# Performance work log

Measured on AMD Instinct MI355X. Metric: run time of the kernel, lower is better.

## Reference

```python
import jax, jax.numpy as jnp
import numpy as np

B, S, D = 2, 1024, 4096
HQ, HKV, HD = 32, 8, 128
GROUPS = HQ // HKV          # 4
SCALE = HD ** -0.5


def _rope_tables(key):
    # standard RoPE cos/sin tables, non-interleaved (half-split) layout
    inv_freq = 1.0 / (10000.0 ** (jnp.arange(0, HD, 2, dtype=jnp.float32) / HD))  # [HD/2]
    pos = jnp.arange(S, dtype=jnp.float32)                                        # [S]
    freqs = pos[:, None] * inv_freq[None, :]                                      # [S, HD/2]
    emb = jnp.concatenate([freqs, freqs], axis=-1)                                # [S, HD]
    cos = jnp.broadcast_to(jnp.cos(emb)[None], (B, S, HD))
    sin = jnp.broadcast_to(jnp.sin(emb)[None], (B, S, HD))
    return cos, sin


def setup_inputs() -> dict:
    key = jax.random.key(0)
    ks = jax.random.split(key, 6)
    hidden_states = jax.random.normal(ks[0], (B, S, D), dtype=jnp.float32)
    cos_table, sin_table = _rope_tables(ks[1])
    Wq = jax.random.normal(ks[2], (D, HQ * HD), dtype=jnp.float32) * (D ** -0.5)
    Wk = jax.random.normal(ks[3], (D, HKV * HD), dtype=jnp.float32) * (D ** -0.5)
    Wv = jax.random.normal(ks[4], (D, HKV * HD), dtype=jnp.float32) * (D ** -0.5)
    Wo = jax.random.normal(ks[5], (HQ * HD, D), dtype=jnp.float32) * ((HQ * HD) ** -0.5)
    return {"hidden_states": hidden_states, "cos_table": cos_table,
            "sin_table": sin_table, "Wq": Wq, "Wk": Wk, "Wv": Wv, "Wo": Wo}


def _rotate_half(x):
    x1, x2 = jnp.split(x, 2, axis=-1)
    return jnp.concatenate([-x2, x1], axis=-1)


def _apply_rope(x, cos, sin):
    # x: [B, S, H, HD]; cos/sin: [B, S, HD] broadcast across heads
    c = cos[:, :, None, :]
    s = sin[:, :, None, :]
    return x * c + _rotate_half(x) * s


def reference(hidden_states, cos_table, sin_table, Wq, Wk, Wv, Wo):
    b, s, _ = hidden_states.shape
    # QKV projections (no bias, Llama-style)
    q = (hidden_states @ Wq).reshape(b, s, HQ, HD)
    k = (hidden_states @ Wk).reshape(b, s, HKV, HD)
    v = (hidden_states @ Wv).reshape(b, s, HKV, HD)
    # fused RoPE on q and k (in [B, S, H, HD] layout, as in source)
    q = _apply_rope(q, cos_table, sin_table)
    k = _apply_rope(k, cos_table, sin_table)
    # -> [B, H, S, HD]
    q = q.transpose(0, 2, 1, 3)
    k = k.transpose(0, 2, 1, 3)
    v = v.transpose(0, 2, 1, 3)
    # GQA repeat_kv: [B, HKV, S, HD] -> [B, HQ, S, HD]
    k = jnp.repeat(k, GROUPS, axis=1)
    v = jnp.repeat(v, GROUPS, axis=1)
    # SDPA, no mask (source calls sdpa without a mask)
    scores = jnp.einsum('bhqd,bhkd->bhqk', q, k) * SCALE
    attn = jax.nn.softmax(scores, axis=-1)
    out = jnp.einsum('bhqk,bhkd->bhqd', attn, v)
    out = out.transpose(0, 2, 1, 3).reshape(b, s, HQ * HD)
    return out @ Wo
```

## Files before the change

### kernel.cpp

```cpp
#include <hip/hip_runtime.h>

#define B_   2
#define S_   1024
#define D_   4096
#define HQ_  32
#define HKV_ 8
#define HD_  128
#define SCALE_ 0.08838834764831845f

typedef unsigned short u16;
typedef __attribute__((ext_vector_type(8))) short s16x8;
typedef __attribute__((ext_vector_type(4))) short s16x4;
typedef __attribute__((ext_vector_type(4))) float f32x4;

#define MFMA(a,b,c) __builtin_amdgcn_mfma_f32_16x16x32_bf16((a),(b),(c),0,0,0)

__device__ __forceinline__ u16 bf16_rne(float x) {
  unsigned u = __float_as_uint(x);
  u += 0x7fffu + ((u >> 16) & 1u);
  return (u16)(u >> 16);
}
__device__ __forceinline__ float bf16_up(u16 h) {
  return __uint_as_float(((unsigned)h) << 16);
}
__device__ __forceinline__ void split2(float x, u16& h, u16& l) {
  h = bf16_rne(x);
  l = bf16_rne(x - bf16_up(h));
}

__device__ __forceinline__ void cvt_hi_lo(float a, float b, unsigned& hi, unsigned& lo) {
  unsigned h, l;
  asm("v_cvt_pk_bf16_f32 %0, %1, %2" : "=v"(h) : "v"(a), "v"(b));
  float ra = __uint_as_float(h << 16);
  float rb = __uint_as_float(h & 0xffff0000u);
  float la = a - ra, lb = b - rb;
  asm("v_cvt_pk_bf16_f32 %0, %1, %2" : "=v"(l) : "v"(la), "v"(lb));
  hi = h; lo = l;
}
__device__ __forceinline__ void pack8(float4 x, float4 y, uint4& h, uint4& l) {
  unsigned h0,h1,h2,h3,l0,l1,l2,l3;
  cvt_hi_lo(x.x, x.y, h0, l0);
  cvt_hi_lo(x.z, x.w, h1, l1);
  cvt_hi_lo(y.x, y.y, h2, l2);
  cvt_hi_lo(y.z, y.w, h3, l3);
  h = make_uint4(h0,h1,h2,h3); l = make_uint4(l0,l1,l2,l3);
}

typedef const __attribute__((address_space(1))) void* gas_ptr;
typedef __attribute__((address_space(3))) void* las_ptr;
__device__ __forceinline__ void gload_lds16(const void* g, void* l) {
  __builtin_amdgcn_global_load_lds((gas_ptr)g, (las_ptr)l, 16, 0, 0);
}

__global__ __launch_bounds__(256) void frag_b(
    const float* __restrict__ W, u16* __restrict__ dh, u16* __restrict__ dl,
    int N, int n0, int Nc16)
{
  __shared__ float T[32][68];
  const int kt = blockIdx.x, nbk = blockIdx.y;
  const int tid = threadIdx.x;
#pragma unroll
  for (int rep = 0; rep < 2; ++rep) {
    int idx = tid + rep * 256;
    int row = idx >> 4, c4 = (idx & 15) * 4;
    float4 v = *reinterpret_cast<const float4*>(&W[(size_t)(kt*32 + row) * N + n0 + nbk*64 + c4]);
    *reinterpret_cast<float4*>(&T[row][c4]) = v;
  }
  __syncthreads();
  const size_t base = ((size_t)kt * Nc16 + nbk * 4) * 512;
  int c = tid;
  int nt = c >> 6, l = c & 63, kc = l >> 4, r = l & 15;
  u16 hh[8], ll[8];
#pragma unroll
  for (int j = 0; j < 8; ++j) split2(T[kc*8 + j][nt*16 + r], hh[j], ll[j]);
  *reinterpret_cast<s16x8*>(&dh[base + (size_t)c * 8]) =
    (s16x8){(short)hh[0],(short)hh[1],(short)hh[2],(short)hh[3],
            (short)hh[4],(short)hh[5],(short)hh[6],(short)hh[7]};
  *reinterpret_cast<s16x8*>(&dl[base + (size_t)c * 8]) =
    (s16x8){(short)ll[0],(short)ll[1],(short)ll[2],(short)ll[3],
            (short)ll[4],(short)ll[5],(short)ll[6],(short)ll[7]};
}

__global__ __launch_bounds__(512) void gemm_p1(
    const float* __restrict__ X, const float* __restrict__ abp,
    const u16* __restrict__ WF,
    float* __restrict__ qb, float* __restrict__ kb, float* __restrict__ vb,
    float* __restrict__ outp, int mode, int col0)
{
  __shared__ __attribute__((aligned(16))) u16 lds[40960];
  u16* ah0 = lds;
  u16* al0 = lds + 4096;
  u16* ah1 = lds + 8192;
  u16* al1 = lds + 12288;
  u16* bh0 = lds + 16384;
  u16* bh1 = lds + 24576;
  u16* blb = lds + 32768;

  const int id   = blockIdx.x;
  const int cpx  = gridDim.x >> 3;
  const int swz  = (id & 7) * cpx + (id >> 3);

  const float* A; const u16* Bh; const u16* Bl; float* C;
  int ldc, Nc16, mb, nb;
  if (mode == 0) {
    if (swz < 128)      { A=X; Bh=WF;          Bl=WF+8388608;  C=qb; ldc=4096; Nc16=128; mb=swz>>3; nb=swz&7; }
    else if (swz < 192) { int u=swz-128; A=X; Bh=WF+16777216; Bl=WF+20971520; C=kb; ldc=1024; Nc16=64; mb=u>>2; nb=u&3; }
    else                { int u=swz-192; A=X; Bh=WF+25165824; Bl=WF+29360128; C=vb; ldc=1024; Nc16=64; mb=u>>2; nb=u&3; }
  } else if (mode == 1) {
    A=X; Bh=WF; Bl=WF+8388608; C=qb+col0; ldc=4096; Nc16=128; mb=swz>>3; nb=swz&7;
  } else if (mode == 2) {
    if (swz < 64) { A=X; Bh=WF;          Bl=WF+4194304;  C=kb; ldc=1024; Nc16=64; mb=swz>>2; nb=swz&3; }
    else          { int u=swz-64; A=X; Bh=WF+8388608; Bl=WF+12582912; C=vb; ldc=1024; Nc16=64; mb=u>>2; nb=u&3; }
  } else if (mode == 3) {
    A=abp; Bh=WF; Bl=WF+16777216; C=outp; ldc=4096; Nc16=256; mb=swz>>4; nb=swz&15;
  } else {
    A=abp; Bh=WF; Bl=WF+8388608; C=outp+col0; ldc=4096; Nc16=128; mb=swz>>3; nb=swz&7;
  }

  const int tid  = threadIdx.x;
  const int lane = tid & 63;
  const int wid  = tid >> 6;
  const int mtb  = (wid >> 2) * 4;
  const int ntb  = (wid & 3) * 4;
  const int loff = lane * 8;

  const int arow = tid >> 2;
  const int akc  = tid & 3;
  const float* aptr = A + (size_t)(mb*128 + arow) * 4096 + akc*8;
  const int awr = (arow >> 4)*512 + (akc*16 + (arow & 15))*8;

  const size_t bStep = (size_t)Nc16 * 512;
  const u16* pBh = Bh + (size_t)nb*16*512 + loff;
  const u16* pBl = Bl + (size_t)nb*16*512 + loff;

  f32x4 acc[4][4];
#pragma unroll
  for (int i = 0; i < 4; ++i)
#pragma unroll
    for (int j = 0; j < 4; ++j) acc[i][j] = (f32x4){0.f, 0.f, 0.f, 0.f};

  float4 ra0 = *reinterpret_cast<const float4*>(aptr);
  float4 ra1 = *reinterpret_cast<const float4*>(aptr + 4);
  {
    uint4 h4, l4; pack8(ra0, ra1, h4, l4);
    *reinterpret_cast<uint4*>(&ah0[awr]) = h4;
    *reinterpret_cast<uint4*>(&al0[awr]) = l4;
  }
  gload_lds16(pBh + (size_t)wid*512,     bh0 + wid*512);
  gload_lds16(pBh + (size_t)(wid+8)*512, bh0 + (wid+8)*512);
  ra0 = *reinterpret_cast<const float4*>(aptr + 32);
  ra1 = *reinterpret_cast<const float4*>(aptr + 36);
  __syncthreads();

  for (int kt = 0; kt < 128; ++kt) {
    u16* cAh = (kt & 1) ? ah1 : ah0;
    u16* cAl = (kt & 1) ? al1 : al0;
    u16* nAh = (kt & 1) ? ah0 : ah1;
    u16* nAl = (kt & 1) ? al0 : al1;
    u16* cBh = (kt & 1) ? bh1 : bh0;
    u16* nBh = (kt & 1) ? bh0 : bh1;

    gload_lds16(pBl + (size_t)kt*bStep + (size_t)wid*512,     blb + wid*512);
    gload_lds16(pBl + (size_t)kt*bStep + (size_t)(wid+8)*512, blb + (wid+8)*512);
    if (kt < 127) {
      gload_lds16(pBh + (size_t)(kt+1)*bStep + (size_t)wid*512,     nBh + wid*512);
      gload_lds16(pBh + (size_t)(kt+1)*bStep + (size_t)(wid+8)*512, nBh + (wid+8)*512);
    }
    s16x8 a_h[4], a_l[4], b_h[4];
#pragma unroll
    for (int mf = 0; mf < 4; ++mf) {
      a_h[mf] = *reinterpret_cast<const s16x8*>(&cAh[(mtb+mf)*512 + loff]);
      a_l[mf] = *reinterpret_cast<const s16x8*>(&cAl[(mtb+mf)*512 + loff]);
    }
#pragma unroll
    for (int nf = 0; nf < 4; ++nf)
      b_h[nf] = *reinterpret_cast<const s16x8*>(&cBh[(ntb+nf)*512 + loff]);
#pragma unroll
    for (int mf = 0; mf < 4; ++mf)
#pragma unroll
      for (int nf = 0; nf < 4; ++nf) {
        acc[mf][nf] = MFMA(a_h[mf], b_h[nf], acc[mf][nf]);
        acc[mf][nf] = MFMA(a_l[mf], b_h[nf], acc[mf][nf]);
      }
    __syncthreads();

    s16x8 b_l[4];
#pragma unroll
    for (int nf = 0; nf < 4; ++nf)
      b_l[nf] = *reinterpret_cast<const s16x8*>(&blb[(ntb+nf)*512 + loff]);
#pragma unroll
    for (int mf = 0; mf < 4; ++mf)
#pragma unroll
      for (int nf = 0; nf < 4; ++nf)
        acc[mf][nf] = MFMA(a_h[mf], b_l[nf], acc[mf][nf]);
    if (kt < 127) {
      uint4 h4, l4; pack8(ra0, ra1, h4, l4);
      *reinterpret_cast<uint4*>(&nAh[awr]) = h4;
      *reinterpret_cast<uint4*>(&nAl[awr]) = l4;
      if (kt < 126) {
        ra0 = *reinterpret_cast<const float4*>(aptr + (kt+2)*32);
        ra1 = *reinterpret_cast<const float4*>(aptr + (kt+2)*32 + 4);
      }
    }
    __syncthreads();
  }

  const int lr = lane & 15, lg = lane >> 4;
  const int row0 = mb*128 + (wid >> 2) * 64;
  const int nloc = nb*256 + (wid & 3) * 64;
#pragma unroll
  for (int mf = 0; mf < 4; ++mf)
#pragma unroll
    for (int nf = 0; nf < 4; ++nf)
#pragma unroll
      for (int r = 0; r < 4; ++r)
        C[(size_t)(row0 + mf*16 + lg*4 + r) * ldc + nloc + nf*16 + lr] = acc[mf][nf][r];
}

__device__ __forceinline__ void gemm_core_128x256(
    const float* __restrict__ A, const float* __restrict__ W,
    float* __restrict__ C, int ldw, int m0, int n0)
{
  __shared__ u16 Ah[128][40];
  __shared__ u16 Al[128][40];
  __shared__ u16 Bh[256][40];
  __shared__ u16 Bl[256][40];

  const int tid  = threadIdx.x;
  const int lane = tid & 63;
  const int wid  = tid >> 6;
  const int wm   = (wid >> 2) * 64;
  const int wn   = (wid & 3) * 64;
  const int lr   = lane & 15;
  const int lg   = lane >> 4;

  f32x4 acc[4][4];
#pragma unroll
  for (int i = 0; i < 4; ++i)
#pragma unroll
    for (int j = 0; j < 4; ++j) acc[i][j] = (f32x4){0.f, 0.f, 0.f, 0.f};

  const int ar  = tid >> 3;
  const int ak  = (tid & 7) * 4;
  const int bn  = tid & 255;
  const int bk0 = (tid >> 8) * 16;

  for (int kt = 0; kt < D_ / 32; ++kt) {
    const int k0 = kt * 32;
    __syncthreads();
#pragma unroll
    for (int j = 0; j < 2; ++j) {
      int r = ar + 64 * j;
      float4 v = *reinterpret_cast<const float4*>(&A[(size_t)(m0 + r) * D_ + k0 + ak]);
      u16 h0,h1,h2,h3,l0,l1,l2,l3;
      split2(v.x,h0,l0); split2(v.y,h1,l1); split2(v.z,h2,l2); split2(v.w,h3,l3);
      *reinterpret_cast<s16x4*>(&Ah[r][ak]) = (s16x4){(short)h0,(short)h1,(short)h2,(short)h3};
      *reinterpret_cast<s16x4*>(&Al[r][ak]) = (s16x4){(short)l0,(short)l1,(short)l2,(short)l3};
    }
    {
      const float* wp = W + (size_t)(k0 + bk0) * ldw + (n0 + bn);
#pragma unroll
      for (int q = 0; q < 4; ++q) {
        float v0 = wp[(q*4 + 0) * (size_t)ldw];
        float v1 = wp[(q*4 + 1) * (size_t)ldw];
        float v2 = wp[(q*4 + 2) * (size_t)ldw];
        float v3 = wp[(q*4 + 3) * (size_t)ldw];
        u16 h0,h1,h2,h3,l0,l1,l2,l3;
        split2(v0,h0,l0); split2(v1,h1,l1); split2(v2,h2,l2); split2(v3,h3,l3);
        *reinterpret_cast<s16x4*>(&Bh[bn][bk0 + q*4]) = (s16x4){(short)h0,(short)h1,(short)h2,(short)h3};
        *reinterpret_cast<s16x4*>(&Bl[bn][bk0 + q*4]) = (s16x4){(short)l0,(short)l1,(short)l2,(short)l3};
      }
    }
    __syncthreads();
    s16x8 a_h[4], a_l[4], b_h[4], b_l[4];
#pragma unroll
    for (int mf = 0; mf < 4; ++mf) {
      a_h[mf] = *reinterpret_cast<const s16x8*>(&Ah[wm + mf*16 + lr][lg*8]);
      a_l[mf] = *reinterpret_cast<const s16x8*>(&Al[wm + mf*16 + lr][lg*8]);
    }
#pragma unroll
    for (int nf = 0; nf < 4; ++nf) {
      b_h[nf] = *reinterpret_cast<const s16x8*>(&Bh[wn + nf*16 + lr][lg*8]);
      b_l[nf] = *reinterpret_cast<const s16x8*>(&Bl[wn + nf*16 + lr][lg*8]);
    }
#pragma unroll
    for (int mf = 0; mf < 4; ++mf)
#pragma unroll
      for (int nf = 0; nf < 4; ++nf) {
        acc[mf][nf] = MFMA(a_h[mf], b_h[nf], acc[mf][nf]);
        acc[mf][nf] = MFMA(a_l[mf], b_h[nf], acc[mf][nf]);
        acc[mf][nf] = MFMA(a_h[mf], b_l[nf], acc[mf][nf]);
      }
  }
#pragma unroll
  for (int mf = 0; mf < 4; ++mf)
#pragma unroll
    for (int nf = 0; nf < 4; ++nf)
#pragma unroll
      for (int r = 0; r < 4; ++r) {
        int row = m0 + wm + mf*16 + lg*4 + r;
        int col = n0 + wn + nf*16 + lr;
        C[(size_t)row * ldw + col] = acc[mf][nf][r];
      }
}

__global__ __launch_bounds__(512) void gemm_qkv_kernel(
    const float* __restrict__ X,
    const float* __restrict__ Wq, const float* __restrict__ Wk,
    const float* __restrict__ Wv,
    float* __restrict__ qb, float* __restrict__ kb, float* __restrict__ vb)
{
  int nbv = blockIdx.x;
  int m0 = blockIdx.y * 128;
  const float* W; float* C; int ldw, n0;
  if (nbv < 16)      { W = Wq; C = qb; ldw = HQ_*HD_;  n0 = nbv * 256; }
  else if (nbv < 20) { W = Wk; C = kb; ldw = HKV_*HD_; n0 = (nbv-16) * 256; }
  else               { W = Wv; C = vb; ldw = HKV_*HD_; n0 = (nbv-20) * 256; }
  gemm_core_128x256(X, W, C, ldw, m0, n0);
}

__global__ __launch_bounds__(512) void gemm_out_kernel(
    const float* __restrict__ A, const float* __restrict__ Wo, float* __restrict__ out)
{
  gemm_core_128x256(A, Wo, out, D_, blockIdx.y * 128, blockIdx.x * 256);
}

__global__ __launch_bounds__(256) void rope_kernel(
    float* __restrict__ qb, float* __restrict__ kb,
    const float* __restrict__ cosT, const float* __restrict__ sinT)
{
  int idx = blockIdx.x * 256 + threadIdx.x;
  const int nq = B_ * S_ * HQ_ * (HD_/2);
  const int nk = B_ * S_ * HKV_ * (HD_/2);
  if (idx < nq) {
    int j = idx & 63;
    int h = (idx >> 6) & (HQ_ - 1);
    int bs = idx >> 11;
    float* p = qb + ((size_t)bs * HQ_ + h) * HD_;
    const float* cp = cosT + (size_t)bs * HD_;
    const float* sp = sinT + (size_t)bs * HD_;
    float x1 = p[j], x2 = p[j + 64];
    p[j]      = x1 * cp[j]      - x2 * sp[j];
    p[j + 64] = x2 * cp[j + 64] + x1 * sp[j + 64];
  } else if (idx < nq + nk) {
    int t2 = idx - nq;
    int j = t2 & 63;
    int h = (t2 >> 6) & (HKV_ - 1);
    int bs = t2 >> 9;
    float* p = kb + ((size_t)bs * HKV_ + h) * HD_;
    const float* cp = cosT + (size_t)bs * HD_;
    const float* sp = sinT + (size_t)bs * HD_;
    float x1 = p[j], x2 = p[j + 64];
    p[j]      = x1 * cp[j]      - x2 * sp[j];
    p[j + 64] = x2 * cp[j + 64] + x1 * sp[j + 64];
  }
}

__global__ __launch_bounds__(512) void attn_kernel(
    const float* __restrict__ qb, const float* __restrict__ kb,
    const float* __restrict__ vb, float* __restrict__ ob)
{
  __shared__ u16 Kh[64][136], Kl[64][136];
  __shared__ u16 Vh[128][72], Vl[128][72];
  __shared__ u16 Ph[8][16][72], Pl[8][16][72];

  const int tid  = threadIdx.x;
  const int lane = tid & 63;
  const int wid  = tid >> 6;
  const int lr   = lane & 15;
  const int lg   = lane >> 4;
  const int qt   = blockIdx.x;
  const int bh   = blockIdx.y;
  const int b    = bh >> 5, h = bh & 31, kvh = h >> 2;

  s16x8 qh[4], ql[4];
  {
    const int qrow = qt * 128 + wid * 16 + lr;
    const float* qp = qb + ((size_t)((b * S_ + qrow) * HQ_ + h)) * HD_;
#pragma unroll
    for (int kc = 0; kc < 4; ++kc) {
      const float* qp2 = qp + kc * 32 + lg * 8;
      float4 v0 = *reinterpret_cast<const float4*>(qp2);
      float4 v1 = *reinterpret_cast<const float4*>(qp2 + 4);
      u16 hh[8], ll[8];
      split2(v0.x,hh[0],ll[0]); split2(v0.y,hh[1],ll[1]);
      split2(v0.z,hh[2],ll[2]); split2(v0.w,hh[3],ll[3]);
      split2(v1.x,hh[4],ll[4]); split2(v1.y,hh[5],ll[5]);
      split2(v1.z,hh[6],ll[6]); split2(v1.w,hh[7],ll[7]);
      qh[kc] = (s16x8){(short)hh[0],(short)hh[1],(short)hh[2],(short)hh[3],
                       (short)hh[4],(short)hh[5],(short)hh[6],(short)hh[7]};
      ql[kc] = (s16x8){(short)ll[0],(short)ll[1],(short)ll[2],(short)ll[3],
                       (short)ll[4],(short)ll[5],(short)ll[6],(short)ll[7]};
    }
  }

  f32x4 acc_o[8];
#pragma unroll
  for (int df = 0; df < 8; ++df) acc_o[df] = (f32x4){0.f, 0.f, 0.f, 0.f};
  float m_run[4] = {-1e30f, -1e30f, -1e30f, -1e30f};
  float l_run[4] = {0.f, 0.f, 0.f, 0.f};

  const float* kbase = kb + ((size_t)(b * S_) * HKV_ + kvh) * HD_;
  const float* vbase = vb + ((size_t)(b * S_) * HKV_ + kvh) * HD_;

  for (int t = 0; t < S_ / 64; ++t) {
    const int kk0 = t * 64;
    __syncthreads();
#pragma unroll
    for (int j = 0; j < 4; ++j) {
      int idx = tid + 512 * j;
      int kk = idx >> 5, dq = (idx & 31) * 4;
      float4 v = *reinterpret_cast<const float4*>(kbase + (size_t)(kk0 + kk) * (HKV_*HD_) + dq);
      u16 h0,h1,h2,h3,l0,l1,l2,l3;
      split2(v.x,h0,l0); split2(v.y,h1,l1); split2(v.z,h2,l2); split2(v.w,h3,l3);
      *reinterpret_cast<s16x4*>(&Kh[kk][dq]) = (s16x4){(short)h0,(short)h1,(short)h2,(short)h3};
      *reinterpret_cast<s16x4*>(&Kl[kk][dq]) = (s16x4){(short)l0,(short)l1,(short)l2,(short)l3};
    }
    {
      int d = tid & 127;
      int kkb = (tid >> 7) * 16;
      const float* vcol = vbase + d;
#pragma unroll
      for (int jq = 0; jq < 4; ++jq) {
        u16 h4[4], l4[4];
#pragma unroll
        for (int e = 0; e < 4; ++e) {
          float val = vcol[(size_t)(kk0 + kkb + jq*4 + e) * (HKV_*HD_)];
          split2(val, h4[e], l4[e]);
        }
        *reinterpret_cast<s16x4*>(&Vh[d][kkb + jq*4]) = (s16x4){(short)h4[0],(short)h4[1],(short)h4[2],(short)h4[3]};
        *reinterpret_cast<s16x4*>(&Vl[d][kkb + jq*4]) = (s16x4){(short)l4[0],(short)l4[1],(short)l4[2],(short)l4[3]};
      }
    }
    __syncthreads();
    f32x4 accs[4];
#pragma unroll
    for (int nf = 0; nf < 4; ++nf) accs[nf] = (f32x4){0.f, 0.f, 0.f, 0.f};
#pragma unroll
    for (int nf = 0; nf < 4; ++nf) {
      int krow = nf * 16 + lr;
#pragma unroll
      for (int kc = 0; kc < 4; ++kc) {
        s16x8 kh8 = *reinterpret_cast<const s16x8*>(&Kh[krow][kc*32 + lg*8]);
        s16x8 kl8 = *reinterpret_cast<const s16x8*>(&Kl[krow][kc*32 + lg*8]);
        accs[nf] = MFMA(qh[kc], kh8, accs[nf]);
        accs[nf] = MFMA(ql[kc], kh8, accs[nf]);
        accs[nf] = MFMA(qh[kc], kl8, accs[nf]);
      }
    }
#pragma unroll
    for (int nf = 0; nf < 4; ++nf) accs[nf] *= SCALE_;
    float corr[4], rsum[4];
#pragma unroll
    for (int r = 0; r < 4; ++r) {
      float t0 = fmaxf(fmaxf(accs[0][r], accs[1][r]), fmaxf(accs[2][r], accs[3][r]));
      t0 = fmaxf(t0, __shfl_xor(t0, 1));
      t0 = fmaxf(t0, __shfl_xor(t0, 2));
      t0 = fmaxf(t0, __shfl_xor(t0, 4));
      t0 = fmaxf(t0, __shfl_xor(t0, 8));
      float mnew = fmaxf(m_run[r], t0);
      corr[r] = __expf(m_run[r] - mnew);
      m_run[r] = mnew;
      rsum[r] = 0.f;
    }
#pragma unroll
    for (int nf = 0; nf < 4; ++nf)
#pragma unroll
      for (int r = 0; r < 4; ++r) {
        float p = __expf(accs[nf][r] - m_run[r]);
        rsum[r] += p;
        u16 ph, pl;
        split2(p, ph, pl);
        Ph[wid][lg*4 + r][nf*16 + lr] = ph;
        Pl[wid][lg*4 + r][nf*16 + lr] = pl;
      }
#pragma unroll
    for (int r = 0; r < 4; ++r) {
      float s = rsum[r];
      s += __shfl_xor(s, 1); s += __shfl_xor(s, 2);
      s += __shfl_xor(s, 4); s += __shfl_xor(s, 8);
      l_run[r] = l_run[r] * corr[r] + s;
    }
#pragma unroll
    for (int df = 0; df < 8; ++df)
#pragma unroll
      for (int r = 0; r < 4; ++r) acc_o[df][r] *= corr[r];
    s16x8 pa_h[2], pa_l[2];
#pragma unroll
    for (int kc = 0; kc < 2; ++kc) {
      pa_h[kc] = *reinterpret_cast<const s16x8*>(&Ph[wid][lr][kc*32 + lg*8]);
      pa_l[kc] = *reinterpret_cast<const s16x8*>(&Pl[wid][lr][kc*32 + lg*8]);
    }
#pragma unroll
    for (int df = 0; df < 8; ++df) {
      int dcol = df * 16 + lr;
#pragma unroll
      for (int kc = 0; kc < 2; ++kc) {
        s16x8 vh8 = *reinterpret_cast<const s16x8*>(&Vh[dcol][kc*32 + lg*8]);
        s16x8 vl8 = *reinterpret_cast<const s16x8*>(&Vl[dcol][kc*32 + lg*8]);
        acc_o[df] = MFMA(pa_h[kc], vh8, acc_o[df]);
        acc_o[df] = MFMA(pa_l[kc], vh8, acc_o[df]);
        acc_o[df] = MFMA(pa_h[kc], vl8, acc_o[df]);
      }
    }
  }
  float inv_l[4];
#pragma unroll
  for (int r = 0; r < 4; ++r) inv_l[r] = 1.f / l_run[r];
#pragma unroll
  for (int df = 0; df < 8; ++df)
#pragma unroll
    for (int r = 0; r < 4; ++r) {
      int row = qt * 128 + wid * 16 + lg * 4 + r;
      ob[((size_t)((b * S_ + row) * HQ_ + h)) * HD_ + df*16 + lr] = acc_o[df][r] * inv_l[r];
    }
}

extern "C" void kernel_launch(void* const* d_in, const int* in_sizes, int n_in,
                              void* d_out, int out_size, void* d_ws, size_t ws_size,
                              hipStream_t stream)
{
  const float* hs   = (const float*)d_in[0];
  const float* cosT = (const float*)d_in[1];
  const float* sinT = (const float*)d_in[2];
  const float* Wq   = (const float*)d_in[3];
  const float* Wk   = (const float*)d_in[4];
  const float* Wv   = (const float*)d_in[5];
  const float* Wo   = (const float*)d_in[6];
  float* out = (float*)d_out;

  float* qb = (float*)d_ws;
  float* kb = qb + 8388608;
  float* vb = kb + 2097152;
  float* ab = vb + 2097152;
  u16*   WF = (u16*)(ab + 8388608);

  const size_t WS144 = 83886080ULL + 67108864ULL;
  const size_t WS112 = 83886080ULL + 33554432ULL;
  int total = B_*S_*HQ_*(HD_/2) + B_*S_*HKV_*(HD_/2);

  if (ws_size >= WS144) {
    frag_b<<<dim3(128,32), 256, 0, stream>>>(Wq, WF,          WF+8388608,  4096, 0,    128);
    frag_b<<<dim3(128,16), 256, 0, stream>>>(Wk, WF+16777216, WF+20971520, 1024, 0,    64);
    frag_b<<<dim3(128,16), 256, 0, stream>>>(Wv, WF+25165824, WF+29360128, 1024, 0,    64);
    gemm_p1<<<256, 512, 0, stream>>>(hs, ab, WF, qb, kb, vb, out, 0, 0);
    frag_b<<<dim3(128,32), 256, 0, stream>>>(Wq, WF,          WF+8388608,  4096, 2048, 128);
    gemm_p1<<<128, 512, 0, stream>>>(hs, ab, WF, qb, kb, vb, out, 1, 2048);
    rope_kernel<<<dim3((total + 255)/256), 256, 0, stream>>>(qb, kb, cosT, sinT);
    attn_kernel<<<dim3(8, 64), 512, 0, stream>>>(qb, kb, vb, ab);
    frag_b<<<dim3(128,64), 256, 0, stream>>>(Wo, WF,          WF+16777216, 4096, 0,    256);
    gemm_p1<<<256, 512, 0, stream>>>(hs, ab, WF, qb, kb, vb, out, 3, 0);
  } else if (ws_size >= WS112) {
    frag_b<<<dim3(128,32), 256, 0, stream>>>(Wq, WF, WF+8388608, 4096, 0, 128);
    gemm_p1<<<128, 512, 0, stream>>>(hs, ab, WF, qb, kb, vb, out, 1, 0);
    frag_b<<<dim3(128,32), 256, 0, stream>>>(Wq, WF, WF+8388608, 4096, 2048, 128);
    gemm_p1<<<128, 512, 0, stream>>>(hs, ab, WF, qb, kb, vb, out, 1, 2048);
    frag_b<<<dim3(128,16), 256, 0, stream>>>(Wk, WF,           WF+4194304,  1024, 0, 64);
    frag_b<<<dim3(128,16), 256, 0, stream>>>(Wv, WF+8388608,   WF+12582912, 1024, 0, 64);
    gemm_p1<<<128, 512, 0, stream>>>(hs, ab, WF, qb, kb, vb, out, 2, 0);
    rope_kernel<<<dim3((total + 255)/256), 256, 0, stream>>>(qb, kb, cosT, sinT);
    attn_kernel<<<dim3(8, 64), 512, 0, stream>>>(qb, kb, vb, ab);
    frag_b<<<dim3(128,32), 256, 0, stream>>>(Wo, WF, WF+8388608, 4096, 0, 128);
    gemm_p1<<<128, 512, 0, stream>>>(hs, ab, WF, qb, kb, vb, out, 4, 0);
    frag_b<<<dim3(128,32), 256, 0, stream>>>(Wo, WF, WF+8388608, 4096, 2048, 128);
    gemm_p1<<<128, 512, 0, stream>>>(hs, ab, WF, qb, kb, vb, out, 4, 2048);
  } else {
    gemm_qkv_kernel<<<dim3(24, 16), 512, 0, stream>>>(hs, Wq, Wk, Wv, qb, kb, vb);
    rope_kernel<<<dim3((total + 255)/256), 256, 0, stream>>>(qb, kb, cosT, sinT);
    attn_kernel<<<dim3(8, 64), 512, 0, stream>>>(qb, kb, vb, ab);
    gemm_out_kernel<<<dim3(16, 16), 512, 0, stream>>>(ab, Wo, out);
  }
}
```

Before: 763.3 us.

## Pre-split K/V into bf16 MFMA fragments and use new attention kernel

Adds a frag_kv kernel that converts roped K and V into hi/lo bf16 pairs laid out in MFMA fragment order. A new attn2 kernel then streams these fragments straight from global memory, with no LDS staging and no per-tile conversion. It runs a split-bf16 three-MFMA flash attention with an online softmax and passes P through a small per-wave LDS buffer. This removes the repeated fp32-to-bf16 splitting of K/V across the four query heads that share each KV head, and the shared-memory tile loads. The cost is an extra kernel launch, extra workspace traffic, and global fragment loads in the inner loop with no block-level reuse.

Result: slower. 1.048 ms (+37.3%).

```diff
diff --git a/kernel.cpp b/kernel.cpp
--- a/kernel.cpp
+++ b/kernel.cpp
@@ -79,6 +79,204 @@
   *reinterpret_cast<s16x8*>(&dl[base + (size_t)c * 8]) =
     (s16x8){(short)ll[0],(short)ll[1],(short)ll[2],(short)ll[3],
             (short)ll[4],(short)ll[5],(short)ll[6],(short)ll[7]};
+}
+
+__global__ __launch_bounds__(256) void frag_kv(
+    const float* __restrict__ kb, const float* __restrict__ vb,
+    u16* __restrict__ KFh, u16* __restrict__ KFl,
+    u16* __restrict__ VFh, u16* __restrict__ VFl)
+{
+  __shared__ float T[32][132];
+  const int bid  = blockIdx.x;
+  const int isV  = bid >> 9;
+  const int bkvh = (bid >> 5) & 15;
+  const int chnk = bid & 31;
+  const int tid  = threadIdx.x;
+  const int b    = bkvh >> 3, kvh = bkvh & 7;
+
+  const float* src = isV ? vb : kb;
+  {
+    int r0 = tid >> 5, c4 = (tid & 31) * 4;
+#pragma unroll
+    for (int it = 0; it < 4; ++it) {
+      int row = r0 + it * 8;
+      float4 v = *reinterpret_cast<const float4*>(
+        &src[(((size_t)(b * S_ + chnk*32 + row)) * HKV_ + kvh) * HD_ + c4]);
+      *reinterpret_cast<float4*>(&T[row][c4]) = v;
+    }
+  }
+  __syncthreads();
+#pragma unroll
+  for (int rep = 0; rep < 2; ++rep) {
+    int c2 = tid + rep * 256;
+    int l = c2 & 63;
+    u16 hh[8], ll[8];
+    if (!isV) {
+      int f = c2 >> 6, st_loc = f >> 2, dt = f & 3;
+#pragma unroll
+      for (int j = 0; j < 8; ++j)
+        split2(T[st_loc*16 + (l & 15)][dt*32 + (l >> 4)*8 + j], hh[j], ll[j]);
+      size_t off = ((size_t)bkvh*64 + chnk*2) * 2048 + (size_t)c2 * 8;
+      *reinterpret_cast<s16x8*>(&KFh[off]) =
+        (s16x8){(short)hh[0],(short)hh[1],(short)hh[2],(short)hh[3],
+                (short)hh[4],(short)hh[5],(short)hh[6],(short)hh[7]};
+      *reinterpret_cast<s16x8*>(&KFl[off]) =
+        (s16x8){(short)ll[0],(short)ll[1],(short)ll[2],(short)ll[3],
+                (short)ll[4],(short)ll[5],(short)ll[6],(short)ll[7]};
+    } else {
+      int dt16 = c2 >> 6;
+#pragma unroll
+      for (int j = 0; j < 8; ++j)
+        split2(T[(l >> 4)*8 + j][dt16*16 + (l & 15)], hh[j], ll[j]);
+      size_t off = ((size_t)bkvh*32 + chnk) * 4096 + (size_t)c2 * 8;
+      *reinterpret_cast<s16x8*>(&VFh[off]) =
+        (s16x8){(short)hh[0],(short)hh[1],(short)hh[2],(short)hh[3],
+                (short)hh[4],(short)hh[5],(short)hh[6],(short)hh[7]};
+      *reinterpret_cast<s16x8*>(&VFl[off]) =
+        (s16x8){(short)ll[0],(short)ll[1],(short)ll[2],(short)ll[3],
+                (short)ll[4],(short)ll[5],(short)ll[6],(short)ll[7]};
+    }
+  }
+}
+
+#define PSTR 68
+__global__ __launch_bounds__(512) void attn2(
+    const float* __restrict__ qb,
+    const u16* __restrict__ KFh, const u16* __restrict__ KFl,
+    const u16* __restrict__ VFh, const u16* __restrict__ VFl,
+    float* __restrict__ ob)
+{
+  __shared__ u16 Ph[8][16][PSTR], Pl[8][16][PSTR];
+
+  const int tid  = threadIdx.x;
+  const int lane = tid & 63;
+  const int wid  = tid >> 6;
+  const int lr   = lane & 15;
+  const int lg   = lane >> 4;
+  const int qt   = blockIdx.x;
+  const int bh   = blockIdx.y;
+  const int b    = bh >> 5, h = bh & 31;
+  const int bkvh = b * 8 + (h >> 2);
+
+  s16x8 qh[4], ql[4];
+  {
+    const int qrow = qt * 128 + wid * 16 + lr;
+    const float* qp = qb + ((size_t)((b * S_ + qrow) * HQ_ + h)) * HD_;
+#pragma unroll
+    for (int kc = 0; kc < 4; ++kc) {
+      const float* qp2 = qp + kc * 32 + lg * 8;
+      float4 v0 = *reinterpret_cast<const float4*>(qp2);
+      float4 v1 = *reinterpret_cast<const float4*>(qp2 + 4);
+      uint4 h4, l4; pack8(v0, v1, h4, l4);
+      qh[kc] = *reinterpret_cast<s16x8*>(&h4);
+      ql[kc] = *reinterpret_cast<s16x8*>(&l4);
+    }
+  }
+
+  f32x4 acc_o[8];
+#pragma unroll
+  for (int df = 0; df < 8; ++df) acc_o[df] = (f32x4){0.f, 0.f, 0.f, 0.f};
+  float m_run[4] = {-1e30f, -1e30f, -1e30f, -1e30f};
+  float l_run[4] = {0.f, 0.f, 0.f, 0.f};
+
+  const u16* pkh = KFh + (size_t)bkvh * 131072 + lane * 8;
+  const u16* pkl = KFl + (size_t)bkvh * 131072 + lane * 8;
+  const u16* pvh = VFh + (size_t)bkvh * 131072 + lane * 8;
+  const u16* pvl = VFl + (size_t)bkvh * 131072 + lane * 8;
+
+  for (int t = 0; t < S_ / 64; ++t) {
+    const size_t kbase = (size_t)t * 8192;
+    const size_t vbase = (size_t)t * 8192;
+
+    f32x4 accs[4];
+#pragma unroll
+    for (int nf = 0; nf < 4; ++nf) {
+      accs[nf] = (f32x4){0.f, 0.f, 0.f, 0.f};
+      s16x8 kh8[4], kl8[4];
+#pragma unroll
+      for (int kc = 0; kc < 4; ++kc) {
+        kh8[kc] = *reinterpret_cast<const s16x8*>(pkh + kbase + nf*2048 + kc*512);
+        kl8[kc] = *reinterpret_cast<const s16x8*>(pkl + kbase + nf*2048 + kc*512);
+      }
+#pragma unroll
+      for (int kc = 0; kc < 4; ++kc) {
+        accs[nf] = MFMA(qh[kc], kh8[kc], accs[nf]);
+        accs[nf] = MFMA(ql[kc], kh8[kc], accs[nf]);
+        accs[nf] = MFMA(qh[kc], kl8[kc], accs[nf]);
+      }
+    }
+#pragma unroll
+    for (int nf = 0; nf < 4; ++nf) accs[nf] *= SCALE_;
+
+    float corr[4], rsum[4];
+#pragma unroll
+    for (int r = 0; r < 4; ++r) {
+      float t0 = fmaxf(fmaxf(accs[0][r], accs[1][r]), fmaxf(accs[2][r], accs[3][r]));
+      t0 = fmaxf(t0, __shfl_xor(t0, 1));
+      t0 = fmaxf(t0, __shfl_xor(t0, 2));
+      t0 = fmaxf(t0, __shfl_xor(t0, 4));
+      t0 = fmaxf(t0, __shfl_xor(t0, 8));
+      float mnew = fmaxf(m_run[r], t0);
+      corr[r] = __expf(m_run[r] - mnew);
+      m_run[r] = mnew;
+      rsum[r] = 0.f;
+    }
+#pragma unroll
+    for (int nf = 0; nf < 4; ++nf)
+#pragma unroll
+      for (int r = 0; r < 4; ++r) {
+        float p = __expf(accs[nf][r] - m_run[r]);
+        rsum[r] += p;
+        u16 ph, pl;
+        split2(p, ph, pl);
+        Ph[wid][lg*4 + r][nf*16 + lr] = ph;
+        Pl[wid][lg*4 + r][nf*16 + lr] = pl;
+      }
+#pragma unroll
+    for (int r = 0; r < 4; ++r) {
+      float s = rsum[r];
+      s += __shfl_xor(s, 1); s += __shfl_xor(s, 2);
+      s += __shfl_xor(s, 4); s += __shfl_xor(s, 8);
+      l_run[r] = l_run[r] * corr[r] + s;
+    }
+#pragma unroll
+    for (int df = 0; df < 8; ++df)
+#pragma unroll
+      for (int r = 0; r < 4; ++r) acc_o[df][r] *= corr[r];
+
+    s16x8 pa_h[2], pa_l[2];
+#pragma unroll
+    for (int kc = 0; kc < 2; ++kc) {
+      pa_h[kc] = *reinterpret_cast<const s16x8*>(&Ph[wid][lr][kc*32 + lg*8]);
+      pa_l[kc] = *reinterpret_cast<const s16x8*>(&Pl[wid][lr][kc*32 + lg*8]);
+    }
+#pragma unroll
+    for (int df = 0; df < 8; ++df) {
+      s16x8 vh8[2], vl8[2];
+#pragma unroll
+      for (int kc = 0; kc < 2; ++kc) {
+        vh8[kc] = *reinterpret_cast<const s16x8*>(pvh + vbase + kc*4096 + df*512);
+        vl8[kc] = *reinterpret_cast<const s16x8*>(pvl + vbase + kc*4096 + df*512);
+      }
+#pragma unroll
+      for (int kc = 0; kc < 2; ++kc) {
+        acc_o[df] = MFMA(pa_h[kc], vh8[kc], acc_o[df]);
+        acc_o[df] = MFMA(pa_l[kc], vh8[kc], acc_o[df]);
+        acc_o[df] = MFMA(pa_h[kc], vl8[kc], acc_o[df]);
+      }
+    }
+  }
+
+  float inv_l[4];
+#pragma unroll
+  for (int r = 0; r < 4; ++r) inv_l[r] = 1.f / l_run[r];
+#pragma unroll
+  for (int df = 0; df < 8; ++df)
+#pragma unroll
+    for (int r = 0; r < 4; ++r) {
+      int row = qt * 128 + wid * 16 + lg * 4 + r;
+      ob[((size_t)((b * S_ + row) * HQ_ + h)) * HD_ + df*16 + lr] = acc_o[df][r] * inv_l[r];
+    }
 }
 
 __global__ __launch_bounds__(512) void gemm_p1(
@@ -539,6 +737,11 @@
   const size_t WS112 = 83886080ULL + 33554432ULL;
   int total = B_*S_*HQ_*(HD_/2) + B_*S_*HKV_*(HD_/2);
 
+  u16* KFh = WF;
+  u16* KFl = WF + 2097152;
+  u16* VFh = WF + 4194304;
+  u16* VFl = WF + 6291456;
+
   if (ws_size >= WS144) {
     frag_b<<<dim3(128,32), 256, 0, stream>>>(Wq, WF,          WF+8388608,  4096, 0,    128);
     frag_b<<<dim3(128,16), 256, 0, stream>>>(Wk, WF+16777216, WF+20971520, 1024, 0,    64);
@@ -547,7 +750,8 @@
     frag_b<<<dim3(128,32), 256, 0, stream>>>(Wq, WF,          WF+8388608,  4096, 2048, 128);
     gemm_p1<<<128, 512, 0, stream>>>(hs, ab, WF, qb, kb, vb, out, 1, 2048);
     rope_kernel<<<dim3((total + 255)/256), 256, 0, stream>>>(qb, kb, cosT, sinT);
-    attn_kernel<<<dim3(8, 64), 512, 0, stream>>>(qb, kb, vb, ab);
+    frag_kv<<<1024, 256, 0, stream>>>(kb, vb, KFh, KFl, VFh, VFl);
+    attn2<<<dim3(8, 64), 512, 0, stream>>>(qb, KFh, KFl, VFh, VFl, ab);
     frag_b<<<dim3(128,64), 256, 0, stream>>>(Wo, WF,          WF+16777216, 4096, 0,    256);
     gemm_p1<<<256, 512, 0, stream>>>(hs, ab, WF, qb, kb, vb, out, 3, 0);
   } else if (ws_size >= WS112) {
@@ -559,7 +763,8 @@
     frag_b<<<dim3(128,16), 256, 0, stream>>>(Wv, WF+8388608,   WF+12582912, 1024, 0, 64);
     gemm_p1<<<128, 512, 0, stream>>>(hs, ab, WF, qb, kb, vb, out, 2, 0);
     rope_kernel<<<dim3((total + 255)/256), 256, 0, stream>>>(qb, kb, cosT, sinT);
-    attn_kernel<<<dim3(8, 64), 512, 0, stream>>>(qb, kb, vb, ab);
+    frag_kv<<<1024, 256, 0, stream>>>(kb, vb, KFh, KFl, VFh, VFl);
+    attn2<<<dim3(8, 64), 512, 0, stream>>>(qb, KFh, KFl, VFh, VFl, ab);
     frag_b<<<dim3(128,32), 256, 0, stream>>>(Wo, WF, WF+8388608, 4096, 0, 128);
     gemm_p1<<<128, 512, 0, stream>>>(hs, ab, WF, qb, kb, vb, out, 4, 0);
     frag_b<<<dim3(128,32), 256, 0, stream>>>(Wo, WF, WF+8388608, 4096, 2048, 128);
```
